# Kernel tuning notes

Hardware: AMD Instinct MI355X
Metric: run time of the kernel (lower is better)

## Reference

```python
import jax, jax.numpy as jnp
import numpy as np

D_MODEL = 128
D_STATE = 16
D_CONV = 4
EXPAND = 2
D_INNER = EXPAND * D_MODEL  # 256
DT_RANK = 8  # ceil(d_model/16)
LSTM_H = 128
FC_H = 128
NUM_CLASSES = 5
IN_CH = 12
B, L = 32, 1024


def setup_inputs() -> dict:
    key = jax.random.key(0)
    ks = jax.random.split(key, 20)
    s = 0.02
    inp = {
        'x': jax.random.normal(ks[0], (B, L, IN_CH), jnp.float32),
        'w_proj': jax.random.normal(ks[1], (D_MODEL, IN_CH), jnp.float32) * s,
        'b_proj': jnp.zeros((D_MODEL,), jnp.float32),
        'w_inproj': jax.random.normal(ks[2], (2 * D_INNER, D_MODEL), jnp.float32) * s,
        'conv_w': jax.random.normal(ks[3], (D_INNER, D_CONV), jnp.float32) * s,
        'conv_b': jnp.zeros((D_INNER,), jnp.float32),
        'w_xproj': jax.random.normal(ks[4], (DT_RANK + 2 * D_STATE, D_INNER), jnp.float32) * s,
        'w_dt': jax.random.normal(ks[5], (D_INNER, DT_RANK), jnp.float32) * s,
        'b_dt': jax.random.normal(ks[6], (D_INNER,), jnp.float32) * s,
        'A_log': jnp.broadcast_to(jnp.log(jnp.arange(1, D_STATE + 1, dtype=jnp.float32)), (D_INNER, D_STATE)).copy(),
        'Dskip': jnp.ones((D_INNER,), jnp.float32),
        'w_out': jax.random.normal(ks[7], (D_MODEL, D_INNER), jnp.float32) * s,
        'w_ih': jax.random.normal(ks[8], (4 * LSTM_H, D_MODEL), jnp.float32) * s,
        'w_hh': jax.random.normal(ks[9], (4 * LSTM_H, LSTM_H), jnp.float32) * s,
        'b_ih': jnp.zeros((4 * LSTM_H,), jnp.float32),
        'b_hh': jnp.zeros((4 * LSTM_H,), jnp.float32),
        'w_fc1': jax.random.normal(ks[10], (FC_H, LSTM_H), jnp.float32) * s,
        'b_fc1': jnp.zeros((FC_H,), jnp.float32),
        'w_fc2': jax.random.normal(ks[11], (NUM_CLASSES, FC_H), jnp.float32) * s,
        'b_fc2': jnp.zeros((NUM_CLASSES,), jnp.float32),
    }
    return inp


def reference(x, w_proj, b_proj, w_inproj, conv_w, conv_b, w_xproj, w_dt, b_dt,
              A_log, Dskip, w_out, w_ih, w_hh, b_ih, b_hh, w_fc1, b_fc1, w_fc2, b_fc2):
    # input projection: (B,L,C) -> (B,L,Dm)
    h = x @ w_proj.T + b_proj
    # ---- Mamba block ----
    xz = h @ w_inproj.T                      # (B,L,2*di)
    u, z = xz[..., :D_INNER], xz[..., D_INNER:]
    # causal depthwise conv1d (kernel D_CONV)
    up = jnp.pad(u, ((0, 0), (D_CONV - 1, 0), (0, 0)))
    u = sum(conv_w[:, k] * up[:, k:k + L, :] for k in range(D_CONV)) + conv_b
    u = jax.nn.silu(u)
    xdbc = u @ w_xproj.T                     # (B,L,dt_rank+2*ds)
    dt = jax.nn.softplus(xdbc[..., :DT_RANK] @ w_dt.T + b_dt)   # (B,L,di)
    Bm = xdbc[..., DT_RANK:DT_RANK + D_STATE]                    # (B,L,ds)
    Cm = xdbc[..., DT_RANK + D_STATE:]                           # (B,L,ds)
    A = -jnp.exp(A_log)                                          # (di,ds)

    def ssm_step(hstate, inp):
        dt_t, B_t, C_t, u_t = inp            # (B,di),(B,ds),(B,ds),(B,di)
        dA = jnp.exp(dt_t[..., None] * A)    # (B,di,ds)
        hstate = hstate * dA + (dt_t * u_t)[..., None] * B_t[:, None, :]
        y_t = jnp.einsum('bds,bs->bd', hstate, C_t)
        return hstate, y_t

    h0 = jnp.zeros((u.shape[0], D_INNER, D_STATE), u.dtype)
    inps = (jnp.swapaxes(dt, 0, 1), jnp.swapaxes(Bm, 0, 1),
            jnp.swapaxes(Cm, 0, 1), jnp.swapaxes(u, 0, 1))
    _, ys = jax.lax.scan(ssm_step, h0, inps)
    y = jnp.swapaxes(ys, 0, 1) + u * Dskip
    y = y * jax.nn.silu(z)
    y = y @ w_out.T                          # (B,L,Dm)
    # ---- LSTM (single layer, batch_first); only last hidden is used ----
    xg = y @ w_ih.T + (b_ih + b_hh)          # (B,L,4H)

    def lstm_step(carry, g_x):
        hh, cc = carry
        g = g_x + hh @ w_hh.T
        i = jax.nn.sigmoid(g[:, :LSTM_H])
        f = jax.nn.sigmoid(g[:, LSTM_H:2 * LSTM_H])
        gg = jnp.tanh(g[:, 2 * LSTM_H:3 * LSTM_H])
        o = jax.nn.sigmoid(g[:, 3 * LSTM_H:])
        cc = f * cc + i * gg
        hh = o * jnp.tanh(cc)
        return (hh, cc), None

    hc0 = (jnp.zeros((y.shape[0], LSTM_H), y.dtype), jnp.zeros((y.shape[0], LSTM_H), y.dtype))
    (h_last, _), _ = jax.lax.scan(lstm_step, hc0, jnp.swapaxes(xg, 0, 1))
    # ---- FC head (dropout is identity in eval) ----
    out = jnp.maximum(h_last @ w_fc1.T + b_fc1, 0.0)
    return out @ w_fc2.T + b_fc2
```

## Files before the change

kernel.cpp:

```cpp
#include <hip/hip_runtime.h>
#include <math.h>

#define Bsz 32
#define Lseq 1024
#define CHUNK 64
#define NCHUNK 16

typedef __attribute__((ext_vector_type(8))) short s16x8v;
typedef __attribute__((ext_vector_type(4))) int   i32x4v;
typedef __attribute__((ext_vector_type(4))) float f32x4v;

__device__ __forceinline__ float fsig(float x) {
    return __builtin_amdgcn_rcpf(1.f + __expf(-x));
}
__device__ __forceinline__ float ftanh(float x) {
    float x2 = x * x;
    float poly = x * (1.f - 0.333333333f * x2 + 0.133333333f * x2 * x2);
    float big = 1.f - 2.f * __builtin_amdgcn_rcpf(1.f + __expf(2.f * x));
    return (x2 < 0.0025f) ? poly : big;
}
__device__ __forceinline__ float fsilu(float x) {
    return x * __builtin_amdgcn_rcpf(1.f + __expf(-x));
}
__device__ __forceinline__ unsigned bfr(float x) {
    unsigned u = __float_as_uint(x);
    return (u + 0x7fffu + ((u >> 16) & 1u)) >> 16;
}
#define BFP(a, b) ( bfr(a) | (bfr(b) << 16) )

__global__ void k_pre(const float* w_proj, const float* b_proj, const float* w_inproj,
                      const float* A_log, const float* w_ih, const float* w_out,
                      const float* b_ih, const float* b_hh,
                      float* Ab, float* Minp, float* cinp, float* M2T, float* c2) {
    int idx = blockIdx.x * 256 + threadIdx.x;
    if (idx < 4096) {
        Ab[idx] = -expf(A_log[idx]);
    } else if (idx < 4096 + 6144) {
        int j = idx - 4096; int o = j / 12; int i = j - o * 12;
        float s = 0.f;
        for (int k = 0; k < 128; ++k) s += w_inproj[o*128+k] * w_proj[k*12+i];
        Minp[j] = s;
    } else if (idx < 4096 + 6144 + 512) {
        int o = idx - (4096 + 6144);
        float s = 0.f;
        for (int k = 0; k < 128; ++k) s += w_inproj[o*128+k] * b_proj[k];
        cinp[o] = s;
    } else if (idx < 4096 + 6144 + 512 + 131072) {
        int j = idx - (4096 + 6144 + 512);
        int o = j >> 8; int dd = j & 255;
        float s = 0.f;
        for (int k = 0; k < 128; ++k) s += w_ih[o*128+k] * w_out[k*256+dd];
        int op = 4*(o & 127) + (o >> 7);
        M2T[dd*512 + op] = s;
    } else if (idx < 4096 + 6144 + 512 + 131072 + 512) {
        int o = idx - (4096 + 6144 + 512 + 131072);
        c2[4*(o & 127) + (o >> 7)] = b_ih[o] + b_hh[o];
    }
}

__global__ void __launch_bounds__(256) k_front(const float* __restrict__ x,
                       const float* __restrict__ Minp, const float* __restrict__ cinp,
                       const float* __restrict__ conv_w, const float* __restrict__ conv_b,
                       float* __restrict__ uc, float* __restrict__ zb) {
    __shared__ float xs[67*12];
    int b = blockIdx.x >> 4;
    int c = blockIdx.x & 15;
    int d = threadIdx.x;
    int t0 = c * 64;
    for (int i = d; i < 67*12; i += 256) {
        int trel = i / 12;
        int t = t0 - 3 + trel;
        xs[i] = (t >= 0) ? x[(b*1024 + t)*12 + (i - trel*12)] : 0.f;
    }
    __syncthreads();
    float mu[12], mz[12];
#pragma unroll
    for (int i = 0; i < 12; ++i) { mu[i] = Minp[d*12 + i]; mz[i] = Minp[(256+d)*12 + i]; }
    float cu = cinp[d], cz = cinp[256 + d];
    float cw0 = conv_w[d*4+0], cw1 = conv_w[d*4+1], cw2 = conv_w[d*4+2], cw3 = conv_w[d*4+3];
    float cb = conv_b[d];
    float r0 = 0.f, r1 = 0.f, r2 = 0.f;
#pragma unroll
    for (int k = 0; k < 3; ++k) {
        int t = t0 - 3 + k;
        float v = 0.f;
        if (t >= 0) {
            const float* xr = &xs[k*12];
            v = cu;
#pragma unroll
            for (int i = 0; i < 12; ++i) v += mu[i]*xr[i];
        }
        r0 = r1; r1 = r2; r2 = v;
    }
    for (int t = t0; t < t0 + 64; ++t) {
        const float* xr = &xs[(t - t0 + 3)*12];
        float u = cu, z = cz;
#pragma unroll
        for (int i = 0; i < 12; ++i) { u += mu[i]*xr[i]; z += mz[i]*xr[i]; }
        float cv = cb + cw0*r0 + cw1*r1 + cw2*r2 + cw3*u;
        uc[(b*1024 + t)*256 + d] = fsilu(cv);
        zb[(b*1024 + t)*256 + d] = z;
        r0 = r1; r1 = r2; r2 = u;
    }
}

__global__ void __launch_bounds__(256) k_xproj(const float* __restrict__ uc,
                        const float* __restrict__ w_xproj, const float* __restrict__ w_dt,
                        const float* __restrict__ b_dt,
                        float* __restrict__ dtb, float* __restrict__ Bm, float* __restrict__ Cm) {
    __shared__ float ur[256];
    __shared__ float xd[40];
    int tok = blockIdx.x;
    int tid = threadIdx.x;
    ur[tid] = uc[tok*256 + tid];
    __syncthreads();
    int j = tid >> 2, q = tid & 3;
    float s = 0.f;
    if (j < 40) {
        const float* wr = w_xproj + j*256 + q*64;
        const float* uq = ur + q*64;
#pragma unroll 8
        for (int k = 0; k < 64; ++k) s += wr[k] * uq[k];
    }
    s += __shfl_xor(s, 1);
    s += __shfl_xor(s, 2);
    if (j < 40 && q == 0) {
        xd[j] = s;
        if (j >= 8 && j < 24)      Bm[tok*16 + (j - 8)]  = s;
        else if (j >= 24)          Cm[tok*16 + (j - 24)] = s;
    }
    __syncthreads();
    float r = b_dt[tid];
    const float* wd = w_dt + tid*8;
#pragma unroll
    for (int jj = 0; jj < 8; ++jj) r += wd[jj] * xd[jj];
    r = (r > 20.f) ? r : log1pf(expf(r));
    dtb[tok*256 + tid] = r;
}

__global__ void __launch_bounds__(256) k_ssm_p1(const float* __restrict__ dtb,
                        const float* __restrict__ uc, const float* __restrict__ Bm,
                        const float* __restrict__ Ab,
                        float* __restrict__ h0end, float* __restrict__ Ssum) {
    __shared__ float Bs[CHUNK*16];
    int b = blockIdx.x >> 4;
    int c = blockIdx.x & 15;
    int d = threadIdx.x;
    int t0 = c * CHUNK;
    {
        const float* src = Bm + (b*1024 + t0) * 16;
        for (int i = d; i < CHUNK*16; i += 256) Bs[i] = src[i];
    }
    __syncthreads();
    float a[16], h[16];
#pragma unroll
    for (int s = 0; s < 16; ++s) { a[s] = Ab[d*16+s]; h[s] = 0.f; }
    float S = 0.f;
    const float* dtp = dtb + (b*1024 + t0)*256 + d;
    const float* up  = uc  + (b*1024 + t0)*256 + d;
    float dtv = dtp[0], uv = up[0];
    for (int t = 0; t < CHUNK; ++t) {
        float dtn = 0.f, un = 0.f;
        if (t < CHUNK-1) { dtn = dtp[(t+1)*256]; un = up[(t+1)*256]; }
        float dtu = dtv * uv;
        S += dtv;
#pragma unroll
        for (int s = 0; s < 16; ++s) {
            float dA = __expf(dtv * a[s]);
            h[s] = h[s]*dA + dtu * Bs[t*16+s];
        }
        dtv = dtn; uv = un;
    }
    float* he = h0end + ((b*256 + d)*16 + c)*16;
#pragma unroll
    for (int s = 0; s < 16; ++s) he[s] = h[s];
    Ssum[(b*256 + d)*16 + c] = S;
}

__global__ void k_ssm_p2(const float* __restrict__ h0end, const float* __restrict__ Ssum,
                         const float* __restrict__ Ab, float* __restrict__ hinit) {
    int gid = blockIdx.x * 256 + threadIdx.x;
    int s = gid & 15;
    int bd = gid >> 4;
    int d = bd & 255;
    float a = Ab[d*16 + s];
    float carry = 0.f;
    const float* he = h0end + bd * 256;
    float* hi = hinit + bd * 256;
    const float* Sp = Ssum + bd * 16;
    for (int c = 0; c < 16; ++c) {
        hi[c*16 + s] = carry;
        carry = he[c*16 + s] + __expf(a * Sp[c]) * carry;
    }
}

__global__ void __launch_bounds__(256) k_ssm_p3(const float* __restrict__ dtb,
                        const float* __restrict__ uc, const float* __restrict__ zb,
                        const float* __restrict__ Bm, const float* __restrict__ Cm,
                        const float* __restrict__ Ab, const float* __restrict__ Dskip,
                        const float* __restrict__ hinit, float* __restrict__ yg) {
    __shared__ float Bs[CHUNK*16];
    __shared__ float Cs[CHUNK*16];
    int b = blockIdx.x >> 4;
    int c = blockIdx.x & 15;
    int d = threadIdx.x;
    int t0 = c * CHUNK;
    {
        const float* srcB = Bm + (b*1024 + t0) * 16;
        const float* srcC = Cm + (b*1024 + t0) * 16;
        for (int i = d; i < CHUNK*16; i += 256) { Bs[i] = srcB[i]; Cs[i] = srcC[i]; }
    }
    __syncthreads();
    float a[16], h[16];
    const float* hi = hinit + ((b*256 + d)*16 + c)*16;
#pragma unroll
    for (int s = 0; s < 16; ++s) { a[s] = Ab[d*16+s]; h[s] = hi[s]; }
    float Dv = Dskip[d];
    const float* dtp = dtb + (b*1024 + t0)*256 + d;
    const float* up  = uc  + (b*1024 + t0)*256 + d;
    const float* zp  = zb  + (b*1024 + t0)*256 + d;
    float* yp = yg + (b*1024 + t0)*256 + d;
    float dtv = dtp[0], uv = up[0], zv = zp[0];
    for (int t = 0; t < CHUNK; ++t) {
        float dtn = 0.f, un = 0.f, zn = 0.f;
        if (t < CHUNK-1) { dtn = dtp[(t+1)*256]; un = up[(t+1)*256]; zn = zp[(t+1)*256]; }
        float dtu = dtv * uv;
        float y = 0.f;
#pragma unroll
        for (int s = 0; s < 16; ++s) {
            float dA = __expf(dtv * a[s]);
            h[s] = h[s]*dA + dtu * Bs[t*16+s];
            y += h[s] * Cs[t*16+s];
        }
        yp[t*256] = (y + uv * Dv) * fsilu(zv);
        dtv = dtn; uv = un; zv = zn;
    }
}

__global__ void __launch_bounds__(256) k_xg(const float* __restrict__ yg,
                      const float* __restrict__ M2T, const float* __restrict__ c2,
                      float* __restrict__ xg) {
    __shared__ float ytile[16][257];
    int tokbase = blockIdx.x * 16;
    int tid = threadIdx.x;
    for (int r = 0; r < 16; ++r) ytile[r][tid] = yg[(tokbase + r)*256 + tid];
    __syncthreads();
    int o0 = tid, o1 = tid + 256;
    float acc0[16], acc1[16];
    float cc0 = c2[o0], cc1 = c2[o1];
#pragma unroll
    for (int r = 0; r < 16; ++r) { acc0[r] = cc0; acc1[r] = cc1; }
#pragma unroll 4
    for (int k = 0; k < 256; ++k) {
        float m0 = M2T[k*512 + o0];
        float m1 = M2T[k*512 + o1];
#pragma unroll
        for (int r = 0; r < 16; ++r) {
            float yv = ytile[r][k];
            acc0[r] = fmaf(yv, m0, acc0[r]);
            acc1[r] = fmaf(yv, m1, acc1[r]);
        }
    }
    for (int r = 0; r < 16; ++r) {
        xg[(tokbase + r)*512 + o0] = acc0[r];
        xg[(tokbase + r)*512 + o1] = acc1[r];
    }
}

#define BAR() asm volatile("s_waitcnt lgkmcnt(0)\ns_barrier" ::: "memory")
#define MKA(m, ks, Av) { \
    int rg = 16*(4*wv + (m)) + col; \
    const float* wr0 = w_hh + ((rg & 3)*128 + (rg >> 2))*128 + (ks)*32 + q*8; \
    i32x4v ti; \
    ti.x = BFP(wr0[0], wr0[1]); ti.y = BFP(wr0[2], wr0[3]); \
    ti.z = BFP(wr0[4], wr0[5]); ti.w = BFP(wr0[6], wr0[7]); \
    Av = __builtin_bit_cast(s16x8v, ti); }
#define RDB(CUR, ks, Bv) { \
    i32x4v ti = *(const i32x4v*)(hl + (CUR)*2176 + col*136 + (ks)*32 + q*8); \
    Bv = __builtin_bit_cast(s16x8v, ti); }
#define TILE_MM(m, Aa, Ab_, Ac, Ad) { \
    f32x4v acc = (f32x4v){0.f, 0.f, 0.f, 0.f}; \
    acc = __builtin_amdgcn_mfma_f32_16x16x32_bf16(Aa,  B0, acc, 0, 0, 0); \
    acc = __builtin_amdgcn_mfma_f32_16x16x32_bf16(Ab_, B1, acc, 0, 0, 0); \
    acc = __builtin_amdgcn_mfma_f32_16x16x32_bf16(Ac,  B2, acc, 0, 0, 0); \
    acc = __builtin_amdgcn_mfma_f32_16x16x32_bf16(Ad,  B3, acc, 0, 0, 0); \
    if (col == 0) *(f32x4v*)(gpre + 64*wv + 16*(m) + 4*q) = acc; \
}
#define STEP2(CUR, NXT, XQ) { \
    s16x8v B0, B1, B2, B3; \
    RDB(CUR, 0, B0) RDB(CUR, 1, B1) RDB(CUR, 2, B2) RDB(CUR, 3, B3) \
    TILE_MM(0, A00, A01, A02, A03) \
    TILE_MM(1, A10, A11, A12, A13) \
    TILE_MM(2, A20, A21, A22, A23) \
    TILE_MM(3, A30, A31, A32, A33) \
    BAR(); \
    float p = gpre[tid] + (XQ); \
    float ye = aa * __builtin_amdgcn_rcpf(1.f + __expf(-sc * p)) + bb; \
    float p2 = p * p; \
    float yp = p * (1.f - 0.333333333f*p2 + 0.133333333f*p2*p2); \
    float act = (gg2 && p2 < 0.0025f) ? yp : ye; \
    float actf = __shfl(act, 1, 4); \
    float actg = __shfl(act, 2, 4); \
    float acto = __shfl(act, 3, 4); \
    if (gid == 0) { \
        cst = actf * cst + act * actg; \
        hreg = acto * ftanh(cst); \
        hl[(NXT)*2176 + uid] = (short)bfr(hreg); \
    } \
    BAR(); \
}

__global__ void __launch_bounds__(512)
k_lstm(const float* __restrict__ xg,
       const float* __restrict__ w_hh,
       const float* __restrict__ w_fc1, const float* __restrict__ b_fc1,
       const float* __restrict__ w_fc2, const float* __restrict__ b_fc2,
       float* __restrict__ out) {
    __shared__ __align__(16) short hl[2*2176];
    __shared__ __align__(16) float gpre[512];
    __shared__ float fcbuf[128];
    __shared__ float relu[128];
    int b = blockIdx.x;
    int tid = threadIdx.x;
    int wv = tid >> 6;
    int l  = tid & 63;
    int col = l & 15;
    int q   = l >> 4;
    int gid = tid & 3;
    int uid = tid >> 2;
    bool gg2 = (gid == 2);
    float sc = gg2 ? 2.f : 1.f;
    float aa = gg2 ? 2.f : 1.f;
    float bb = gg2 ? -1.f : 0.f;
    s16x8v A00,A01,A02,A03, A10,A11,A12,A13, A20,A21,A22,A23, A30,A31,A32,A33;
    MKA(0,0,A00) MKA(0,1,A01) MKA(0,2,A02) MKA(0,3,A03)
    MKA(1,0,A10) MKA(1,1,A11) MKA(1,2,A12) MKA(1,3,A13)
    MKA(2,0,A20) MKA(2,1,A21) MKA(2,2,A22) MKA(2,3,A23)
    MKA(3,0,A30) MKA(3,1,A31) MKA(3,2,A32) MKA(3,3,A33)
    for (int i = tid; i < 2*2176; i += 512) hl[i] = 0;
    __syncthreads();
    float cst = 0.f, hreg = 0.f;
    const float* xqp = xg + (size_t)b * 1024 * 512 + tid;
    float xqa = xqp[0];
    float xqb = xqp[512];
    for (int t = 0; t < 1024; t += 2) {
        float xa = xqa, xb = xqb;
        if (t + 2 < 1024) { xqa = xqp[(size_t)(t+2)*512]; xqb = xqp[(size_t)(t+3)*512]; }
        STEP2(0, 1, xa)
        STEP2(1, 0, xb)
    }
    if (gid == 0) fcbuf[uid] = hreg;
    __syncthreads();
    if (tid < 128) {
        float s = b_fc1[tid];
        const float* wf = w_fc1 + tid*128;
#pragma unroll 4
        for (int k = 0; k < 128; ++k) s += wf[k] * fcbuf[k];
        relu[tid] = fmaxf(s, 0.f);
    }
    __syncthreads();
    if (tid < 5) {
        float s = b_fc2[tid];
        const float* wf = w_fc2 + tid*128;
        for (int k = 0; k < 128; ++k) s += wf[k] * relu[k];
        out[b*5 + tid] = s;
    }
}

extern "C" void kernel_launch(void* const* d_in, const int* in_sizes, int n_in,
                              void* d_out, int out_size, void* d_ws, size_t ws_size,
                              hipStream_t stream) {
    const float* x        = (const float*)d_in[0];
    const float* w_proj   = (const float*)d_in[1];
    const float* b_proj   = (const float*)d_in[2];
    const float* w_inproj = (const float*)d_in[3];
    const float* conv_w   = (const float*)d_in[4];
    const float* conv_b   = (const float*)d_in[5];
    const float* w_xproj  = (const float*)d_in[6];
    const float* w_dt     = (const float*)d_in[7];
    const float* b_dt     = (const float*)d_in[8];
    const float* A_log    = (const float*)d_in[9];
    const float* Dskip    = (const float*)d_in[10];
    const float* w_out    = (const float*)d_in[11];
    const float* w_ih     = (const float*)d_in[12];
    const float* w_hh     = (const float*)d_in[13];
    const float* b_ih     = (const float*)d_in[14];
    const float* b_hh     = (const float*)d_in[15];
    const float* w_fc1    = (const float*)d_in[16];
    const float* b_fc1    = (const float*)d_in[17];
    const float* w_fc2    = (const float*)d_in[18];
    const float* b_fc2    = (const float*)d_in[19];
    float* outp = (float*)d_out;

    float* ws = (float*)d_ws;
    size_t off = 0;
    float* uc   = ws + off; off += 8388608;
    float* zb   = ws + off; off += 8388608;
    float* dtb  = ws + off; off += 8388608;
    float* yg   = ws + off; off += 8388608;
    float* Bm   = ws + off; off += 524288;
    float* Cm   = ws + off; off += 524288;
    float* Ab   = ws + off; off += 4096;
    float* Minp = ws + off; off += 6144;
    float* cinp = ws + off; off += 512;
    float* M2T  = ws + off; off += 131072;
    float* c2   = ws + off; off += 512;
    float* h0end = ws + off; off += 2097152;
    float* Ssum  = ws + off; off += 131072;
    float* hinit = ws + off; off += 2097152;
    float* xg = uc;

    k_pre<<<556, 256, 0, stream>>>(w_proj, b_proj, w_inproj, A_log, w_ih, w_out,
                                   b_ih, b_hh, Ab, Minp, cinp, M2T, c2);
    k_front<<<512, 256, 0, stream>>>(x, Minp, cinp, conv_w, conv_b, uc, zb);
    k_xproj<<<32768, 256, 0, stream>>>(uc, w_xproj, w_dt, b_dt, dtb, Bm, Cm);
    k_ssm_p1<<<512, 256, 0, stream>>>(dtb, uc, Bm, Ab, h0end, Ssum);
    k_ssm_p2<<<512, 256, 0, stream>>>(h0end, Ssum, Ab, hinit);
    k_ssm_p3<<<512, 256, 0, stream>>>(dtb, uc, zb, Bm, Cm, Ab, Dskip, hinit, yg);
    k_xg<<<2048, 256, 0, stream>>>(yg, M2T, c2, xg);
    k_lstm<<<32, 512, 0, stream>>>(xg, w_hh, w_fc1, b_fc1, w_fc2, b_fc2, outp);
}
```

Baseline: 1.051 ms.

## Use bf16 MFMA for LSTM input-gate GEMM with prepacked weights

The fp32 scalar-FMA GEMM computing the LSTM input gates from the SSM output is replaced by bf16 MFMA 16x16x32 tiles. The fused weight matrix is prepacked into the MFMA operand layout in the setup kernel, and the SSM pass now writes its output as bf16, which halves that intermediate's memory traffic. The cost is bf16 rounding on both activations and weights in a large reduction feeding the LSTM, which risks accuracy.

```diff
diff --git a/kernel.cpp b/kernel.cpp
--- a/kernel.cpp
+++ b/kernel.cpp
@@ -31,7 +31,8 @@
 __global__ void k_pre(const float* w_proj, const float* b_proj, const float* w_inproj,
                       const float* A_log, const float* w_ih, const float* w_out,
                       const float* b_ih, const float* b_hh,
-                      float* Ab, float* Minp, float* cinp, float* M2T, float* c2) {
+                      float* Ab, float* Minp, float* cinp,
+                      unsigned short* M2p, float* c2) {
     int idx = blockIdx.x * 256 + threadIdx.x;
     if (idx < 4096) {
         Ab[idx] = -expf(A_log[idx]);
@@ -51,7 +52,9 @@
         float s = 0.f;
         for (int k = 0; k < 128; ++k) s += w_ih[o*128+k] * w_out[k*256+dd];
         int op = 4*(o & 127) + (o >> 7);
-        M2T[dd*512 + op] = s;
+        int col = op & 15, nt = op >> 4;
+        int ks = dd >> 5, q = (dd >> 3) & 3, jj = dd & 7;
+        M2p[(((nt*8 + ks)*64) + (q*16 + col))*8 + jj] = (unsigned short)bfr(s);
     } else if (idx < 4096 + 6144 + 512 + 131072 + 512) {
         int o = idx - (4096 + 6144 + 512 + 131072);
         c2[4*(o & 127) + (o >> 7)] = b_ih[o] + b_hh[o];
@@ -198,7 +201,7 @@
                         const float* __restrict__ uc, const float* __restrict__ zb,
                         const float* __restrict__ Bm, const float* __restrict__ Cm,
                         const float* __restrict__ Ab, const float* __restrict__ Dskip,
-                        const float* __restrict__ hinit, float* __restrict__ yg) {
+                        const float* __restrict__ hinit, unsigned short* __restrict__ ygb) {
     __shared__ float Bs[CHUNK*16];
     __shared__ float Cs[CHUNK*16];
     int b = blockIdx.x >> 4;
@@ -219,7 +222,7 @@
     const float* dtp = dtb + (b*1024 + t0)*256 + d;
     const float* up  = uc  + (b*1024 + t0)*256 + d;
     const float* zp  = zb  + (b*1024 + t0)*256 + d;
-    float* yp = yg + (b*1024 + t0)*256 + d;
+    unsigned short* yp = ygb + (b*1024 + t0)*256 + d;
     float dtv = dtp[0], uv = up[0], zv = zp[0];
     for (int t = 0; t < CHUNK; ++t) {
         float dtn = 0.f, un = 0.f, zn = 0.f;
@@ -232,38 +235,49 @@
             h[s] = h[s]*dA + dtu * Bs[t*16+s];
             y += h[s] * Cs[t*16+s];
         }
-        yp[t*256] = (y + uv * Dv) * fsilu(zv);
+        yp[t*256] = (unsigned short)bfr((y + uv * Dv) * fsilu(zv));
         dtv = dtn; uv = un; zv = zn;
     }
 }
 
-__global__ void __launch_bounds__(256) k_xg(const float* __restrict__ yg,
-                      const float* __restrict__ M2T, const float* __restrict__ c2,
+#define XGA(ks, Av) { \
+    i32x4v ti = *(const i32x4v*)(ygb + (size_t)(tokbase + col)*256 + (ks)*32 + q*8); \
+    Av = __builtin_bit_cast(s16x8v, ti); }
+__global__ void __launch_bounds__(256) k_xg(const unsigned short* __restrict__ ygb,
+                      const unsigned short* __restrict__ M2p, const float* __restrict__ c2,
                       float* __restrict__ xg) {
-    __shared__ float ytile[16][257];
-    int tokbase = blockIdx.x * 16;
     int tid = threadIdx.x;
-    for (int r = 0; r < 16; ++r) ytile[r][tid] = yg[(tokbase + r)*256 + tid];
-    __syncthreads();
-    int o0 = tid, o1 = tid + 256;
-    float acc0[16], acc1[16];
-    float cc0 = c2[o0], cc1 = c2[o1];
-#pragma unroll
-    for (int r = 0; r < 16; ++r) { acc0[r] = cc0; acc1[r] = cc1; }
-#pragma unroll 4
-    for (int k = 0; k < 256; ++k) {
-        float m0 = M2T[k*512 + o0];
-        float m1 = M2T[k*512 + o1];
-#pragma unroll
-        for (int r = 0; r < 16; ++r) {
-            float yv = ytile[r][k];
-            acc0[r] = fmaf(yv, m0, acc0[r]);
-            acc1[r] = fmaf(yv, m1, acc1[r]);
-        }
-    }
-    for (int r = 0; r < 16; ++r) {
-        xg[(tokbase + r)*512 + o0] = acc0[r];
-        xg[(tokbase + r)*512 + o1] = acc1[r];
+    int wv = tid >> 6;
+    int l  = tid & 63;
+    int col = l & 15;
+    int q   = l >> 4;
+    int tokbase = blockIdx.x * 64 + wv * 16;
+    s16x8v A0, A1, A2, A3, A4, A5, A6, A7;
+    XGA(0, A0) XGA(1, A1) XGA(2, A2) XGA(3, A3)
+    XGA(4, A4) XGA(5, A5) XGA(6, A6) XGA(7, A7)
+    for (int nt = 0; nt < 32; ++nt) {
+        const i32x4v* bp = (const i32x4v*)(M2p + (size_t)(nt*8)*512 + l*8);
+        f32x4v acc = (f32x4v){0.f, 0.f, 0.f, 0.f};
+        s16x8v B0 = __builtin_bit_cast(s16x8v, bp[0*64]);
+        s16x8v B1 = __builtin_bit_cast(s16x8v, bp[1*64]);
+        s16x8v B2 = __builtin_bit_cast(s16x8v, bp[2*64]);
+        s16x8v B3 = __builtin_bit_cast(s16x8v, bp[3*64]);
+        s16x8v B4 = __builtin_bit_cast(s16x8v, bp[4*64]);
+        s16x8v B5 = __builtin_bit_cast(s16x8v, bp[5*64]);
+        s16x8v B6 = __builtin_bit_cast(s16x8v, bp[6*64]);
+        s16x8v B7 = __builtin_bit_cast(s16x8v, bp[7*64]);
+        acc = __builtin_amdgcn_mfma_f32_16x16x32_bf16(A0, B0, acc, 0, 0, 0);
+        acc = __builtin_amdgcn_mfma_f32_16x16x32_bf16(A1, B1, acc, 0, 0, 0);
+        acc = __builtin_amdgcn_mfma_f32_16x16x32_bf16(A2, B2, acc, 0, 0, 0);
+        acc = __builtin_amdgcn_mfma_f32_16x16x32_bf16(A3, B3, acc, 0, 0, 0);
+        acc = __builtin_amdgcn_mfma_f32_16x16x32_bf16(A4, B4, acc, 0, 0, 0);
+        acc = __builtin_amdgcn_mfma_f32_16x16x32_bf16(A5, B5, acc, 0, 0, 0);
+        acc = __builtin_amdgcn_mfma_f32_16x16x32_bf16(A6, B6, acc, 0, 0, 0);
+        acc = __builtin_amdgcn_mfma_f32_16x16x32_bf16(A7, B7, acc, 0, 0, 0);
+        float cc = c2[nt*16 + col];
+#pragma unroll
+        for (int r = 0; r < 4; ++r)
+            xg[(size_t)(tokbase + q*4 + r)*512 + nt*16 + col] = acc[r] + cc;
     }
 }
 
@@ -397,26 +411,28 @@
     float* uc   = ws + off; off += 8388608;
     float* zb   = ws + off; off += 8388608;
     float* dtb  = ws + off; off += 8388608;
-    float* yg   = ws + off; off += 8388608;
+    float* ygf  = ws + off; off += 8388608;
     float* Bm   = ws + off; off += 524288;
     float* Cm   = ws + off; off += 524288;
     float* Ab   = ws + off; off += 4096;
     float* Minp = ws + off; off += 6144;
     float* cinp = ws + off; off += 512;
-    float* M2T  = ws + off; off += 131072;
+    float* M2f  = ws + off; off += 131072;
     float* c2   = ws + off; off += 512;
     float* h0end = ws + off; off += 2097152;
     float* Ssum  = ws + off; off += 131072;
     float* hinit = ws + off; off += 2097152;
     float* xg = uc;
+    unsigned short* ygb = (unsigned short*)ygf;
+    unsigned short* M2p = (unsigned short*)M2f;
 
     k_pre<<<556, 256, 0, stream>>>(w_proj, b_proj, w_inproj, A_log, w_ih, w_out,
-                                   b_ih, b_hh, Ab, Minp, cinp, M2T, c2);
+                                   b_ih, b_hh, Ab, Minp, cinp, M2p, c2);
     k_front<<<512, 256, 0, stream>>>(x, Minp, cinp, conv_w, conv_b, uc, zb);
     k_xproj<<<32768, 256, 0, stream>>>(uc, w_xproj, w_dt, b_dt, dtb, Bm, Cm);
     k_ssm_p1<<<512, 256, 0, stream>>>(dtb, uc, Bm, Ab, h0end, Ssum);
     k_ssm_p2<<<512, 256, 0, stream>>>(h0end, Ssum, Ab, hinit);
-    k_ssm_p3<<<512, 256, 0, stream>>>(dtb, uc, zb, Bm, Cm, Ab, Dskip, hinit, yg);
-    k_xg<<<2048, 256, 0, stream>>>(yg, M2T, c2, xg);
+    k_ssm_p3<<<512, 256, 0, stream>>>(dtb, uc, zb, Bm, Cm, Ab, Dskip, hinit, ygb);
+    k_xg<<<512, 256, 0, stream>>>(ygb, M2p, c2, xg);
     k_lstm<<<32, 512, 0, stream>>>(xg, w_hh, w_fc1, b_fc1, w_fc2, b_fc2, outp);
 }
```

New measurement: 948.4 us. 1.11x faster.
